# Optimization experiments

Hardware: AMD Instinct MI355X
Metric: run time of the kernel (lower is better)

## Reference

```python
import jax, jax.numpy as jnp
import numpy as np

N, DIM, H = 2048, 512, 8
D = DIM // H  # head dim = 64; M (value head dim) also 64
EPS = 1e-6


def setup_inputs() -> dict:
    key = jax.random.key(0)
    ks = jax.random.split(key, 11)
    s = 1.0 / np.sqrt(DIM)
    return {
        "query": jax.random.normal(ks[0], (N, DIM), dtype=jnp.float32),
        "key": jax.random.normal(ks[1], (N, DIM), dtype=jnp.float32),
        "value": jax.random.normal(ks[2], (N, DIM), dtype=jnp.float32),
        "Si": jax.random.uniform(ks[3], (N, H, D, D), dtype=jnp.float32),
        "Zi": jax.random.uniform(ks[4], (N, H, D), dtype=jnp.float32),
        "Wq": jax.random.uniform(ks[5], (DIM, DIM), minval=-s, maxval=s, dtype=jnp.float32),
        "bq": jax.random.uniform(ks[6], (DIM,), minval=-s, maxval=s, dtype=jnp.float32),
        "Wk": jax.random.uniform(ks[7], (DIM, DIM), minval=-s, maxval=s, dtype=jnp.float32),
        "bk": jax.random.uniform(ks[8], (DIM,), minval=-s, maxval=s, dtype=jnp.float32),
        "Wv": jax.random.uniform(ks[9], (DIM, DIM), minval=-s, maxval=s, dtype=jnp.float32),
        "bv": jax.random.uniform(ks[10], (DIM,), minval=-s, maxval=s, dtype=jnp.float32),
    }


def reference(query, key, value, Si, Zi, Wq, bq, Wk, bk, Wv, bv):
    n = query.shape[0]
    # projections + elu+1 feature map, split into heads: [n, H, D]
    Q = jax.nn.elu(query @ Wq.T + bq).reshape(n, H, D) + 1.0
    K = jax.nn.elu(key @ Wk.T + bk).reshape(n, H, D) + 1.0
    V = jax.nn.elu(value @ Wv.T + bv).reshape(n, H, D) + 1.0  # placeholder line replaced below
    # NOTE: original applies elu only to Q and K; V is the raw projection.
    V = (value @ Wv.T + bv).reshape(n, H, D)
    # state update: running key sum and outer-product accumulator
    Zi_new = Zi + K                                     # [n, H, D]
    Si_new = Si + jnp.einsum('nhd,nhm->nhdm', K, V)     # [n, H, D, M]
    # normalized query-state contraction
    Z = 1.0 / (jnp.einsum('nhd,nhd->nh', Q, Zi_new) + EPS)
    out = jnp.einsum('nhd,nhdm,nh->nhm', Q, Si_new, Z).reshape(n, DIM)
    return out, Si_new, Zi_new
```

## Files before the change

### kernel.cpp

```cpp
#include <hip/hip_runtime.h>
#include <cstdint>
#include <cstddef>

#define NTOK 2048
#define DIMSZ 512
#define NH 8
#define DH 64

typedef __attribute__((ext_vector_type(8))) short bf16x8;
typedef __attribute__((ext_vector_type(4))) float f32x4;

__device__ __forceinline__ short f2bf(float f) {
  uint32_t u = __float_as_uint(f);
  u += 0x7fffu + ((u >> 16) & 1u);
  return (short)(u >> 16);
}

#define LDSS 40

__global__ __launch_bounds__(256) void proj_kernel(
    const float* __restrict__ query, const float* __restrict__ keyi,
    const float* __restrict__ val,
    const float* __restrict__ Wq, const float* __restrict__ bq,
    const float* __restrict__ Wk, const float* __restrict__ bk,
    const float* __restrict__ Wv, const float* __restrict__ bv,
    float* __restrict__ Qp, float* __restrict__ Kp, float* __restrict__ Vp)
{
  const float* A; const float* W; const float* bias; float* P; bool do_elu;
  if (blockIdx.z == 0)      { A = query; W = Wq; bias = bq; P = Qp; do_elu = true; }
  else if (blockIdx.z == 1) { A = keyi;  W = Wk; bias = bk; P = Kp; do_elu = true; }
  else                      { A = val;   W = Wv; bias = bv; P = Vp; do_elu = false; }

  __shared__ short Ash[64 * LDSS];
  __shared__ short Wsh[64 * LDSS];

  const int tid  = threadIdx.x;
  const int lane = tid & 63;
  const int wave = tid >> 6;
  const int l15  = lane & 15;
  const int quad = lane >> 4;
  const int waveM = wave >> 1;
  const int waveN = wave & 1;

  const int rowBase = blockIdx.y * 64;
  const int colBase = blockIdx.x * 64;

  f32x4 acc[2][2] = {};

  const int sRow = tid >> 3;
  const int sCol = (tid & 7) * 4;

  for (int k0 = 0; k0 < DIMSZ; k0 += 32) {
#pragma unroll
    for (int rr = 0; rr < 2; ++rr) {
      const int r = sRow + rr * 32;
      float4 va = *(const float4*)&A[(size_t)(rowBase + r) * DIMSZ + k0 + sCol];
      short4 sa = make_short4(f2bf(va.x), f2bf(va.y), f2bf(va.z), f2bf(va.w));
      *(short4*)&Ash[r * LDSS + sCol] = sa;
      float4 vw = *(const float4*)&W[(size_t)(colBase + r) * DIMSZ + k0 + sCol];
      short4 sw = make_short4(f2bf(vw.x), f2bf(vw.y), f2bf(vw.z), f2bf(vw.w));
      *(short4*)&Wsh[r * LDSS + sCol] = sw;
    }
    __syncthreads();

    bf16x8 afrag[2], bfrag[2];
#pragma unroll
    for (int mi = 0; mi < 2; ++mi) {
      const int m = waveM * 32 + mi * 16 + l15;
      afrag[mi] = *(const bf16x8*)&Ash[m * LDSS + quad * 8];
    }
#pragma unroll
    for (int ni = 0; ni < 2; ++ni) {
      const int n = waveN * 32 + ni * 16 + l15;
      bfrag[ni] = *(const bf16x8*)&Wsh[n * LDSS + quad * 8];
    }
#pragma unroll
    for (int mi = 0; mi < 2; ++mi)
#pragma unroll
      for (int ni = 0; ni < 2; ++ni)
        acc[mi][ni] = __builtin_amdgcn_mfma_f32_16x16x32_bf16(
            afrag[mi], bfrag[ni], acc[mi][ni], 0, 0, 0);
    __syncthreads();
  }

#pragma unroll
  for (int mi = 0; mi < 2; ++mi) {
#pragma unroll
    for (int ni = 0; ni < 2; ++ni) {
      const int gcol = colBase + waveN * 32 + ni * 16 + l15;
      const float b = bias[gcol];
#pragma unroll
      for (int r = 0; r < 4; ++r) {
        const int grow = rowBase + waveM * 32 + mi * 16 + quad * 4 + r;
        float y = acc[mi][ni][r] + b;
        if (do_elu) y = (y > 0.0f) ? (y + 1.0f) : __expf(y);
        P[(size_t)grow * DIMSZ + gcol] = y;
      }
    }
  }
}

__global__ __launch_bounds__(256) void stream_kernel(
    const float* __restrict__ Si, const float* __restrict__ Zi,
    const float* __restrict__ Qp, const float* __restrict__ Kp,
    const float* __restrict__ Vp,
    float* __restrict__ out, float* __restrict__ si_out,
    float* __restrict__ zi_out)
{
  const int wave = threadIdx.x >> 6;
  const int lane = threadIdx.x & 63;
  const int pair = blockIdx.x * 4 + wave;
  const int n = pair >> 3;
  const int h = pair & 7;
  const int l = lane & 15;
  const int g = lane >> 4;

  const int    qkv_off = n * DIMSZ + h * DH;
  const int    zi_off  = pair * DH;
  const size_t si_off  = (size_t)pair * (DH * DH);

  const float4 q4  = *(const float4*)&Qp[qkv_off + l * 4];
  const float4 k4  = *(const float4*)&Kp[qkv_off + l * 4];
  const float4 v4  = *(const float4*)&Vp[qkv_off + l * 4];
  const float4 zi4 = *(const float4*)&Zi[zi_off + l * 4];

  f32x4 zin4;
  zin4.x = zi4.x + k4.x; zin4.y = zi4.y + k4.y;
  zin4.z = zi4.z + k4.z; zin4.w = zi4.w + k4.w;
  if (g == 0)
    __builtin_nontemporal_store(zin4, (f32x4*)&zi_out[zi_off + l * 4]);

  float p = q4.x * zin4.x + q4.y * zin4.y + q4.z * zin4.z + q4.w * zin4.w;
  p += __shfl_xor(p, 1);
  p += __shfl_xor(p, 2);
  p += __shfl_xor(p, 4);
  p += __shfl_xor(p, 8);
  const float z = 1.0f / (p + 1e-6f);

  float qd[16], kd[16];
#pragma unroll
  for (int i = 0; i < 16; ++i) {
    const int d = i * 4 + g;
    qd[i] = Qp[qkv_off + d];
    kd[i] = Kp[qkv_off + d];
  }

  const float* sip = &Si[si_off + (size_t)g * DH + l * 4];
  float*       sop = &si_out[si_off + (size_t)g * DH + l * 4];

  f32x4 s[16];
#pragma unroll
  for (int i = 0; i < 16; ++i)
    s[i] = __builtin_nontemporal_load((const f32x4*)(sip + (size_t)i * 256));

  float a0 = 0.f, a1 = 0.f, a2 = 0.f, a3 = 0.f;
#pragma unroll
  for (int i = 0; i < 16; ++i) {
    f32x4 sn;
    sn.x = s[i].x + kd[i] * v4.x;
    sn.y = s[i].y + kd[i] * v4.y;
    sn.z = s[i].z + kd[i] * v4.z;
    sn.w = s[i].w + kd[i] * v4.w;
    __builtin_nontemporal_store(sn, (f32x4*)(sop + (size_t)i * 256));
    a0 += qd[i] * sn.x;
    a1 += qd[i] * sn.y;
    a2 += qd[i] * sn.z;
    a3 += qd[i] * sn.w;
  }

  a0 += __shfl_xor(a0, 16); a0 += __shfl_xor(a0, 32);
  a1 += __shfl_xor(a1, 16); a1 += __shfl_xor(a1, 32);
  a2 += __shfl_xor(a2, 16); a2 += __shfl_xor(a2, 32);
  a3 += __shfl_xor(a3, 16); a3 += __shfl_xor(a3, 32);

  if (g == 0) {
    float4 o;
    o.x = a0 * z; o.y = a1 * z; o.z = a2 * z; o.w = a3 * z;
    *(float4*)&out[(size_t)n * DIMSZ + h * DH + l * 4] = o;
  }
}

extern "C" void kernel_launch(void* const* d_in, const int* in_sizes, int n_in,
                              void* d_out, int out_size, void* d_ws, size_t ws_size,
                              hipStream_t stream) {
  const float* query = (const float*)d_in[0];
  const float* key_  = (const float*)d_in[1];
  const float* value = (const float*)d_in[2];
  const float* Si    = (const float*)d_in[3];
  const float* Zi    = (const float*)d_in[4];
  const float* Wq    = (const float*)d_in[5];
  const float* bq    = (const float*)d_in[6];
  const float* Wk    = (const float*)d_in[7];
  const float* bk    = (const float*)d_in[8];
  const float* Wv    = (const float*)d_in[9];
  const float* bv    = (const float*)d_in[10];

  float* out    = (float*)d_out;
  float* si_out = out + (size_t)NTOK * DIMSZ;
  float* zi_out = si_out + (size_t)NTOK * NH * DH * DH;

  float* Qp = (float*)d_ws;
  float* Kp = Qp + (size_t)NTOK * DIMSZ;
  float* Vp = Kp + (size_t)NTOK * DIMSZ;

  dim3 g1(DIMSZ / 64, NTOK / 64, 3);
  proj_kernel<<<g1, 256, 0, stream>>>(query, key_, value, Wq, bq, Wk, bk,
                                      Wv, bv, Qp, Kp, Vp);

  stream_kernel<<<NTOK * NH / 4, 256, 0, stream>>>(Si, Zi, Qp, Kp, Vp,
                                                   out, si_out, zi_out);
}
```

Baseline: 488.5 us.

## Fuse QKV projection and state update into a single kernel

Merges the projection GEMM and the streaming Si/Zi update into one kernel. Each block projects 8 tokens across half the heads and keeps Q/K/V in LDS, so the global workspace round trip and the second launch go away. Each block now re-reads half of all three weight matrices (768 rows by 512), which adds a lot of L2 traffic: the 512 blocks pull about 400MB of weights in total. The MFMA M dimension is also only 8 rows per matrix, so half of each 16-row tile is wasted, and the swizzled LDS layout adds complexity.

```diff
diff --git a/kernel.cpp b/kernel.cpp
--- a/kernel.cpp
+++ b/kernel.cpp
@@ -16,167 +16,172 @@
   return (short)(u >> 16);
 }
 
-#define LDSS 40
-
-__global__ __launch_bounds__(256) void proj_kernel(
+__global__ __launch_bounds__(256) void fused_kernel(
     const float* __restrict__ query, const float* __restrict__ keyi,
     const float* __restrict__ val,
+    const float* __restrict__ Si, const float* __restrict__ Zi,
     const float* __restrict__ Wq, const float* __restrict__ bq,
     const float* __restrict__ Wk, const float* __restrict__ bk,
     const float* __restrict__ Wv, const float* __restrict__ bv,
-    float* __restrict__ Qp, float* __restrict__ Kp, float* __restrict__ Vp)
+    float* __restrict__ out, float* __restrict__ si_out,
+    float* __restrict__ zi_out)
 {
-  const float* A; const float* W; const float* bias; float* P; bool do_elu;
-  if (blockIdx.z == 0)      { A = query; W = Wq; bias = bq; P = Qp; do_elu = true; }
-  else if (blockIdx.z == 1) { A = keyi;  W = Wk; bias = bk; P = Kp; do_elu = true; }
-  else                      { A = val;   W = Wv; bias = bv; P = Vp; do_elu = false; }
-
-  __shared__ short Ash[64 * LDSS];
-  __shared__ short Wsh[64 * LDSS];
+  __shared__ short Ash[24 * 520];
+  __shared__ short Wsh[768 * 32];
 
   const int tid  = threadIdx.x;
   const int lane = tid & 63;
   const int wave = tid >> 6;
   const int l15  = lane & 15;
   const int quad = lane >> 4;
-  const int waveM = wave >> 1;
-  const int waveN = wave & 1;
-
-  const int rowBase = blockIdx.y * 64;
-  const int colBase = blockIdx.x * 64;
-
-  f32x4 acc[2][2] = {};
-
-  const int sRow = tid >> 3;
-  const int sCol = (tid & 7) * 4;
-
-  for (int k0 = 0; k0 < DIMSZ; k0 += 32) {
-#pragma unroll
-    for (int rr = 0; rr < 2; ++rr) {
-      const int r = sRow + rr * 32;
-      float4 va = *(const float4*)&A[(size_t)(rowBase + r) * DIMSZ + k0 + sCol];
-      short4 sa = make_short4(f2bf(va.x), f2bf(va.y), f2bf(va.z), f2bf(va.w));
-      *(short4*)&Ash[r * LDSS + sCol] = sa;
-      float4 vw = *(const float4*)&W[(size_t)(colBase + r) * DIMSZ + k0 + sCol];
-      short4 sw = make_short4(f2bf(vw.x), f2bf(vw.y), f2bf(vw.z), f2bf(vw.w));
-      *(short4*)&Wsh[r * LDSS + sCol] = sw;
+
+  const int hg = blockIdx.x >> 8;
+  const int nc = blockIdx.x & 255;
+  const int n0 = nc * 8;
+
+#pragma unroll
+  for (int j = 0; j < 12; ++j) {
+    const int m   = j >> 2;
+    const int rem = (j & 3) * 256 + tid;
+    const int row = rem >> 7;
+    const int c4  = rem & 127;
+    const float* src = (m == 0) ? query : ((m == 1) ? keyi : val);
+    float4 v = *(const float4*)&src[(size_t)(n0 + row) * DIMSZ + c4 * 4];
+    short4 s4 = make_short4(f2bf(v.x), f2bf(v.y), f2bf(v.z), f2bf(v.w));
+    *(short4*)&Ash[(m * 8 + row) * 520 + c4 * 4] = s4;
+  }
+
+  f32x4 acc[12] = {};
+
+  for (int ks = 0; ks < 16; ++ks) {
+    const int k0 = ks * 32;
+#pragma unroll
+    for (int rr = 0; rr < 24; ++rr) {
+      const int r  = rr * 32 + (tid >> 3);
+      const int m  = rr >> 3;
+      const float* wb = (m == 0) ? Wq : ((m == 1) ? Wk : Wv);
+      const int cm = hg * 256 + (r & 255);
+      const int c  = (tid & 7) * 4;
+      float4 v = *(const float4*)&wb[(size_t)cm * DIMSZ + k0 + c];
+      short4 s4 = make_short4(f2bf(v.x), f2bf(v.y), f2bf(v.z), f2bf(v.w));
+      const int bo  = c * 2;
+      const int bos = ((((bo >> 4) ^ ((r >> 1) & 3)) & 3) << 4) | (bo & 8);
+      *(short4*)((char*)Wsh + r * 64 + bos) = s4;
     }
     __syncthreads();
 
-    bf16x8 afrag[2], bfrag[2];
-#pragma unroll
-    for (int mi = 0; mi < 2; ++mi) {
-      const int m = waveM * 32 + mi * 16 + l15;
-      afrag[mi] = *(const bf16x8*)&Ash[m * LDSS + quad * 8];
-    }
-#pragma unroll
-    for (int ni = 0; ni < 2; ++ni) {
-      const int n = waveN * 32 + ni * 16 + l15;
-      bfrag[ni] = *(const bf16x8*)&Wsh[n * LDSS + quad * 8];
-    }
-#pragma unroll
-    for (int mi = 0; mi < 2; ++mi)
-#pragma unroll
-      for (int ni = 0; ni < 2; ++ni)
-        acc[mi][ni] = __builtin_amdgcn_mfma_f32_16x16x32_bf16(
-            afrag[mi], bfrag[ni], acc[mi][ni], 0, 0, 0);
+    bf16x8 af0 = *(const bf16x8*)&Ash[(0 * 8 + (l15 & 7)) * 520 + k0 + quad * 8];
+    bf16x8 af1 = *(const bf16x8*)&Ash[(1 * 8 + (l15 & 7)) * 520 + k0 + quad * 8];
+    bf16x8 af2 = *(const bf16x8*)&Ash[(2 * 8 + (l15 & 7)) * 520 + k0 + quad * 8];
+
+#pragma unroll
+    for (int ntl = 0; ntl < 12; ++ntl) {
+      const int nt = ntl * 4 + wave;
+      const int rB = nt * 16 + l15;
+      const int bos = ((quad ^ ((rB >> 1) & 3)) & 3) << 4;
+      bf16x8 bf = *(const bf16x8*)((const char*)Wsh + rB * 64 + bos);
+      const int m = ntl >> 2;
+      bf16x8 afr = (m == 0) ? af0 : ((m == 1) ? af1 : af2);
+      acc[ntl] = __builtin_amdgcn_mfma_f32_16x16x32_bf16(afr, bf, acc[ntl],
+                                                         0, 0, 0);
+    }
     __syncthreads();
   }
 
-#pragma unroll
-  for (int mi = 0; mi < 2; ++mi) {
-#pragma unroll
-    for (int ni = 0; ni < 2; ++ni) {
-      const int gcol = colBase + waveN * 32 + ni * 16 + l15;
-      const float b = bias[gcol];
+  float* Pl = (float*)Wsh;
+#pragma unroll
+  for (int ntl = 0; ntl < 12; ++ntl) {
+    const int nt  = ntl * 4 + wave;
+    const int m   = ntl >> 2;
+    const int col = nt * 16 + l15;
+    const float* bptr = (m == 0) ? bq : ((m == 1) ? bk : bv);
+    const float bias = bptr[hg * 256 + (col & 255)];
+    if (quad < 2) {
 #pragma unroll
       for (int r = 0; r < 4; ++r) {
-        const int grow = rowBase + waveM * 32 + mi * 16 + quad * 4 + r;
-        float y = acc[mi][ni][r] + b;
-        if (do_elu) y = (y > 0.0f) ? (y + 1.0f) : __expf(y);
-        P[(size_t)grow * DIMSZ + gcol] = y;
-      }
-    }
-  }
-}
-
-__global__ __launch_bounds__(256) void stream_kernel(
-    const float* __restrict__ Si, const float* __restrict__ Zi,
-    const float* __restrict__ Qp, const float* __restrict__ Kp,
-    const float* __restrict__ Vp,
-    float* __restrict__ out, float* __restrict__ si_out,
-    float* __restrict__ zi_out)
-{
-  const int wave = threadIdx.x >> 6;
-  const int lane = threadIdx.x & 63;
-  const int pair = blockIdx.x * 4 + wave;
-  const int n = pair >> 3;
-  const int h = pair & 7;
-  const int l = lane & 15;
-  const int g = lane >> 4;
-
-  const int    qkv_off = n * DIMSZ + h * DH;
-  const int    zi_off  = pair * DH;
-  const size_t si_off  = (size_t)pair * (DH * DH);
-
-  const float4 q4  = *(const float4*)&Qp[qkv_off + l * 4];
-  const float4 k4  = *(const float4*)&Kp[qkv_off + l * 4];
-  const float4 v4  = *(const float4*)&Vp[qkv_off + l * 4];
-  const float4 zi4 = *(const float4*)&Zi[zi_off + l * 4];
-
-  f32x4 zin4;
-  zin4.x = zi4.x + k4.x; zin4.y = zi4.y + k4.y;
-  zin4.z = zi4.z + k4.z; zin4.w = zi4.w + k4.w;
-  if (g == 0)
-    __builtin_nontemporal_store(zin4, (f32x4*)&zi_out[zi_off + l * 4]);
-
-  float p = q4.x * zin4.x + q4.y * zin4.y + q4.z * zin4.z + q4.w * zin4.w;
-  p += __shfl_xor(p, 1);
-  p += __shfl_xor(p, 2);
-  p += __shfl_xor(p, 4);
-  p += __shfl_xor(p, 8);
-  const float z = 1.0f / (p + 1e-6f);
-
-  float qd[16], kd[16];
-#pragma unroll
-  for (int i = 0; i < 16; ++i) {
-    const int d = i * 4 + g;
-    qd[i] = Qp[qkv_off + d];
-    kd[i] = Kp[qkv_off + d];
-  }
-
-  const float* sip = &Si[si_off + (size_t)g * DH + l * 4];
-  float*       sop = &si_out[si_off + (size_t)g * DH + l * 4];
-
-  f32x4 s[16];
-#pragma unroll
-  for (int i = 0; i < 16; ++i)
-    s[i] = __builtin_nontemporal_load((const f32x4*)(sip + (size_t)i * 256));
-
-  float a0 = 0.f, a1 = 0.f, a2 = 0.f, a3 = 0.f;
-#pragma unroll
-  for (int i = 0; i < 16; ++i) {
-    f32x4 sn;
-    sn.x = s[i].x + kd[i] * v4.x;
-    sn.y = s[i].y + kd[i] * v4.y;
-    sn.z = s[i].z + kd[i] * v4.z;
-    sn.w = s[i].w + kd[i] * v4.w;
-    __builtin_nontemporal_store(sn, (f32x4*)(sop + (size_t)i * 256));
-    a0 += qd[i] * sn.x;
-    a1 += qd[i] * sn.y;
-    a2 += qd[i] * sn.z;
-    a3 += qd[i] * sn.w;
-  }
-
-  a0 += __shfl_xor(a0, 16); a0 += __shfl_xor(a0, 32);
-  a1 += __shfl_xor(a1, 16); a1 += __shfl_xor(a1, 32);
-  a2 += __shfl_xor(a2, 16); a2 += __shfl_xor(a2, 32);
-  a3 += __shfl_xor(a3, 16); a3 += __shfl_xor(a3, 32);
-
-  if (g == 0) {
-    float4 o;
-    o.x = a0 * z; o.y = a1 * z; o.z = a2 * z; o.w = a3 * z;
-    *(float4*)&out[(size_t)n * DIMSZ + h * DH + l * 4] = o;
+        const int row = quad * 4 + r;
+        float y = acc[ntl][r] + bias;
+        if (m < 2) y = (y > 0.0f) ? (y + 1.0f) : __expf(y);
+        Pl[row * 768 + col] = y;
+      }
+    }
+  }
+  __syncthreads();
+
+  const int l = l15;
+  const int g = quad;
+
+#pragma unroll
+  for (int ii = 0; ii < 2; ++ii) {
+    const int i = wave * 2 + ii;
+    const int n = n0 + i;
+#pragma unroll
+    for (int hh = 0; hh < 4; ++hh) {
+      const int h    = hg * 4 + hh;
+      const int pair = n * 8 + h;
+      const int    zi_off = pair * DH;
+      const size_t si_off = (size_t)pair * (DH * DH);
+      const int    pbase  = i * 768 + hh * 64;
+
+      const f32x4 q4 = *(const f32x4*)&Pl[pbase + l * 4];
+      const f32x4 k4 = *(const f32x4*)&Pl[pbase + 256 + l * 4];
+      const f32x4 v4 = *(const f32x4*)&Pl[pbase + 512 + l * 4];
+      const float4 zi4 = *(const float4*)&Zi[zi_off + l * 4];
+
+      f32x4 zin4;
+      zin4.x = zi4.x + k4.x; zin4.y = zi4.y + k4.y;
+      zin4.z = zi4.z + k4.z; zin4.w = zi4.w + k4.w;
+      if (g == 0)
+        __builtin_nontemporal_store(zin4, (f32x4*)&zi_out[zi_off + l * 4]);
+
+      float p = q4.x * zin4.x + q4.y * zin4.y + q4.z * zin4.z + q4.w * zin4.w;
+      p += __shfl_xor(p, 1);
+      p += __shfl_xor(p, 2);
+      p += __shfl_xor(p, 4);
+      p += __shfl_xor(p, 8);
+      const float z = 1.0f / (p + 1e-6f);
+
+      float qd[16], kd[16];
+#pragma unroll
+      for (int jj = 0; jj < 16; ++jj) {
+        qd[jj] = Pl[pbase + jj * 4 + g];
+        kd[jj] = Pl[pbase + 256 + jj * 4 + g];
+      }
+
+      const float* sip = &Si[si_off + (size_t)g * DH + l * 4];
+      float*       sop = &si_out[si_off + (size_t)g * DH + l * 4];
+
+      f32x4 s[16];
+#pragma unroll
+      for (int jj = 0; jj < 16; ++jj)
+        s[jj] = __builtin_nontemporal_load((const f32x4*)(sip + (size_t)jj * 256));
+
+      float a0 = 0.f, a1 = 0.f, a2 = 0.f, a3 = 0.f;
+#pragma unroll
+      for (int jj = 0; jj < 16; ++jj) {
+        f32x4 sn;
+        sn.x = s[jj].x + kd[jj] * v4.x;
+        sn.y = s[jj].y + kd[jj] * v4.y;
+        sn.z = s[jj].z + kd[jj] * v4.z;
+        sn.w = s[jj].w + kd[jj] * v4.w;
+        __builtin_nontemporal_store(sn, (f32x4*)(sop + (size_t)jj * 256));
+        a0 += qd[jj] * sn.x;
+        a1 += qd[jj] * sn.y;
+        a2 += qd[jj] * sn.z;
+        a3 += qd[jj] * sn.w;
+      }
+
+      a0 += __shfl_xor(a0, 16); a0 += __shfl_xor(a0, 32);
+      a1 += __shfl_xor(a1, 16); a1 += __shfl_xor(a1, 32);
+      a2 += __shfl_xor(a2, 16); a2 += __shfl_xor(a2, 32);
+      a3 += __shfl_xor(a3, 16); a3 += __shfl_xor(a3, 32);
+
+      if (g == 0) {
+        float4 o;
+        o.x = a0 * z; o.y = a1 * z; o.z = a2 * z; o.w = a3 * z;
+        *(float4*)&out[(size_t)n * DIMSZ + h * DH + l * 4] = o;
+      }
+    }
   }
 }
 
@@ -199,14 +204,7 @@
   float* si_out = out + (size_t)NTOK * DIMSZ;
   float* zi_out = si_out + (size_t)NTOK * NH * DH * DH;
 
-  float* Qp = (float*)d_ws;
-  float* Kp = Qp + (size_t)NTOK * DIMSZ;
-  float* Vp = Kp + (size_t)NTOK * DIMSZ;
-
-  dim3 g1(DIMSZ / 64, NTOK / 64, 3);
-  proj_kernel<<<g1, 256, 0, stream>>>(query, key_, value, Wq, bq, Wk, bk,
-                                      Wv, bv, Qp, Kp, Vp);
-
-  stream_kernel<<<NTOK * NH / 4, 256, 0, stream>>>(Si, Zi, Qp, Kp, Vp,
-                                                   out, si_out, zi_out);
+  fused_kernel<<<512, 256, 0, stream>>>(query, key_, value, Si, Zi,
+                                        Wq, bq, Wk, bk, Wv, bv,
+                                        out, si_out, zi_out);
 }
```

New measurement: 662.2 us. 1.36x slower.
